# Performance work log

Hardware: AMD Instinct MI355X
Metric: run time of the kernel (lower is better)

## Reference

```python
import jax, jax.numpy as jnp
import numpy as np

DIM = 512
HEADS = 8
DIM_HEAD = 64
SCALE = DIM_HEAD ** -0.5


def setup_inputs() -> dict:
    key = jax.random.key(0)
    k1, k2, k3, k4, k5 = jax.random.split(key, 5)
    inner = HEADS * DIM_HEAD
    x = jax.random.normal(k1, (16, DIM, 32, 32), dtype=jnp.float32)
    W_proj = jax.random.normal(k2, (DIM, inner * 3), dtype=jnp.float32) * (DIM ** -0.5)
    b_proj = jax.random.normal(k3, (inner * 3,), dtype=jnp.float32) * 0.01
    W_out = jax.random.normal(k4, (inner, DIM), dtype=jnp.float32) * (inner ** -0.5)
    b_out = jax.random.normal(k5, (DIM,), dtype=jnp.float32) * 0.01
    return {"x": x, "W_proj": W_proj, "b_proj": b_proj, "W_out": W_out, "b_out": b_out}


def reference(x, W_proj, b_proj, W_out, b_out):
    b, c, hh, ww = x.shape
    s = hh * ww
    xs = x.reshape(b, c, s).transpose(0, 2, 1)  # b s c
    qkv = xs @ W_proj + b_proj                  # b s (heads * 3*dim_head)
    qkv = qkv.reshape(b, s, HEADS, 3 * DIM_HEAD)
    q, k, v = jnp.split(qkv, 3, axis=-1)        # each: b s h d
    w = jnp.einsum('bshd,bthd->bsth', q, k) * SCALE
    w = jax.nn.softmax(w, axis=2)
    res = jnp.einsum('bsth,bthd->bshd', w, v).reshape(b, s, HEADS * DIM_HEAD)
    out = res @ W_out + b_out + xs              # b s c (residual)
    return out.transpose(0, 2, 1).reshape(b, c, hh, ww)
```

## Files before the change

### kernel.cpp

```cpp
#include <hip/hip_runtime.h>
#include <hip/hip_bf16.h>

#define BATCH 16
#define CDIM  512
#define SEQ   1024
#define HEADS 8
#define DHEAD 64
#define N3    1536
#define QSCALE 0.18033688011112042f

typedef unsigned short ushort_t;
typedef __attribute__((ext_vector_type(8))) short short8;
typedef __attribute__((ext_vector_type(4))) float f32x4;

__device__ __forceinline__ unsigned f2bf(float f) {
    unsigned u = __float_as_uint(f);
    u += 0x7fffu + ((u >> 16) & 1u);
    return u >> 16;
}
__device__ __forceinline__ float fast_exp2(float x) {
    float r;
    asm("v_exp_f32 %0, %1" : "=v"(r) : "v"(x));
    return r;
}
__device__ __forceinline__ unsigned pack_bf16_trunc(float lo, float hi) {
    return __builtin_amdgcn_perm(__float_as_uint(hi), __float_as_uint(lo), 0x07060302u);
}
__device__ __forceinline__ void async16(const void* g, void* l) {
    __builtin_amdgcn_global_load_lds(
        (const __attribute__((address_space(1))) unsigned int*)g,
        (__attribute__((address_space(3))) unsigned int*)l, 16, 0, 0);
}


__global__ __launch_bounds__(256) void blockify_kernel(
    const float* __restrict__ in, ushort_t* __restrict__ out, int C)
{
    __shared__ float t[64][65];
    const int k0 = blockIdx.y * 64, c0 = blockIdx.x * 64;
    const float* inb = in + (size_t)blockIdx.z * 512 * C;
    const int tid = threadIdx.x;
#pragma unroll
    for (int i = 0; i < 16; ++i) {
        int idx = tid + i * 256;
        int r = idx >> 6, c = idx & 63;
        t[r][c] = inb[(size_t)(k0 + r) * C + c0 + c];
    }
    __syncthreads();
    const size_t mbase = (size_t)blockIdx.z * C + c0;
    const int ml = tid & 63;
#pragma unroll
    for (int i = 0; i < 2; ++i) {
        int oct = (tid >> 6) + i * 4;
        size_t m = mbase + ml;
        int mt = (int)(m >> 7), mr = (int)(m & 127);
        int m16 = mr >> 4, col = mr & 15;
        int k = k0 + oct * 8;
        int it = k >> 5, q = (k >> 3) & 3;
        uint4 pk;
        pk.x = f2bf(t[oct * 8 + 0][ml]) | (f2bf(t[oct * 8 + 1][ml]) << 16);
        pk.y = f2bf(t[oct * 8 + 2][ml]) | (f2bf(t[oct * 8 + 3][ml]) << 16);
        pk.z = f2bf(t[oct * 8 + 4][ml]) | (f2bf(t[oct * 8 + 5][ml]) << 16);
        pk.w = f2bf(t[oct * 8 + 6][ml]) | (f2bf(t[oct * 8 + 7][ml]) << 16);
        size_t off = ((size_t)(mt * 16 + it) * 8 + m16) * 512 + (q * 16 + col) * 8;
        *(uint4*)&out[off] = pk;
    }
}

__global__ __launch_bounds__(256) void qkv_gemm_kernel(
    const ushort_t* __restrict__ xtb, const ushort_t* __restrict__ WpTb,
    const float* __restrict__ bp,
    ushort_t* __restrict__ q_buf, ushort_t* __restrict__ kb,
    ushort_t* __restrict__ vb)
{
    __shared__ alignas(16) ushort_t Asub[2][8 * 512];
    __shared__ alignas(16) ushort_t Bsub[2][8 * 512];

    const int tid = threadIdx.x, w = tid >> 6, lane = tid & 63;
    const int quad = lane >> 4, col = lane & 15;
    const int wm = w >> 1, wn = w & 1;

    const int lin = blockIdx.x + 12 * blockIdx.y;
    const int xcd = lin & 7;
    const int rr  = lin >> 3;
    const int n0  = (rr % 12) * 128;
    const int m0  = ((rr / 12) * 8 + xcd) * 128;

    f32x4 acc[4][4];
#pragma unroll
    for (int i = 0; i < 4; ++i)
#pragma unroll
        for (int j = 0; j < 4; ++j) acc[i][j] = (f32x4){0.f, 0.f, 0.f, 0.f};

    const ushort_t* Ab = xtb  + (size_t)(m0 >> 7) * 65536 + (w * 2) * 512 + lane * 8;
    const ushort_t* Bb = WpTb + (size_t)(n0 >> 7) * 65536 + (w * 2) * 512 + lane * 8;

#define QKV_STAGE(buf, it)                                        \
    do {                                                          \
        async16(Ab + (it) * 4096,       &Asub[buf][(w * 2 + 0) * 512]); \
        async16(Ab + (it) * 4096 + 512, &Asub[buf][(w * 2 + 1) * 512]); \
        async16(Bb + (it) * 4096,       &Bsub[buf][(w * 2 + 0) * 512]); \
        async16(Bb + (it) * 4096 + 512, &Bsub[buf][(w * 2 + 1) * 512]); \
    } while (0)

    QKV_STAGE(0, 0);
    for (int it = 0; it < 16; ++it) {
        const int cur = it & 1;
        __syncthreads();
        if (it < 15) QKV_STAGE(cur ^ 1, it + 1);

        short8 af[4], bfr[4];
#pragma unroll
        for (int i = 0; i < 4; ++i) af[i]  = *(const short8*)&Asub[cur][(wm * 4 + i) * 512 + lane * 8];
#pragma unroll
        for (int j = 0; j < 4; ++j) bfr[j] = *(const short8*)&Bsub[cur][(wn * 4 + j) * 512 + lane * 8];
#pragma unroll
        for (int i = 0; i < 4; ++i)
#pragma unroll
            for (int j = 0; j < 4; ++j)
                acc[i][j] = __builtin_amdgcn_mfma_f32_16x16x32_bf16(af[i], bfr[j], acc[i][j], 0, 0, 0);
    }
#undef QKV_STAGE

    const int b = m0 >> 10, s0 = m0 & 1023;
    const size_t b8 = (size_t)b * HEADS;
#pragma unroll
    for (int j = 0; j < 4; ++j) {
        int nb = n0 + wn * 64 + j * 16;
        int h = nb / 192, rem = nb % 192;
        int type = rem >> 6, dbase = rem & 63;
        float bias = bp[nb + col];
        size_t bh = b8 + h;
        int d = dbase + col;
#pragma unroll
        for (int i = 0; i < 4; ++i) {
            int sb = s0 + wm * 64 + i * 16 + quad * 4;
            f32x4 v = acc[i][j];
            if (type == 2) {
                unsigned lo = f2bf(v[0] + bias) | (f2bf(v[1] + bias) << 16);
                unsigned hi = f2bf(v[2] + bias) | (f2bf(v[3] + bias) << 16);
                uint2 pk; pk.x = lo; pk.y = hi;
                int itv = sb >> 6, sub = (d >> 4) * 2 + ((sb >> 5) & 1);
                size_t off = ((bh * 16 + itv) * 8 + sub) * 512
                           + (((sb >> 3) & 3) * 16 + (d & 15)) * 8 + (sb & 7);
                *(uint2*)&vb[off] = pk;
            } else if (type == 1) {
#pragma unroll
                for (int r = 0; r < 4; ++r) {
                    int t = sb + r;
                    int itk = t >> 6, sub = ((t >> 4) & 3) * 2 + (d >> 5);
                    size_t off = ((bh * 16 + itk) * 8 + sub) * 512
                               + (((d >> 3) & 3) * 16 + (t & 15)) * 8 + (d & 7);
                    kb[off] = (ushort_t)f2bf(v[r] + bias);
                }
            } else {
#pragma unroll
                for (int r = 0; r < 4; ++r)
                    q_buf[(bh * SEQ + sb + r) * DHEAD + d] =
                        (ushort_t)f2bf((v[r] + bias) * QSCALE);
            }
        }
    }
}

__global__ __launch_bounds__(256) void attn_kernel(
    const ushort_t* __restrict__ q_buf, const ushort_t* __restrict__ kb,
    const ushort_t* __restrict__ vb, ushort_t* __restrict__ resb)
{
    __shared__ alignas(16) ushort_t Kf[2][8 * 512];
    __shared__ alignas(16) ushort_t Vf[2][8 * 512];
    __shared__ alignas(16) ushort_t Pf[4 * 1024];

    const int tid  = threadIdx.x;
    const int w    = tid >> 6;
    const int lane = tid & 63;
    const int quad = lane >> 4;
    const int col  = lane & 15;

    const int bhid = blockIdx.x;
    const int b = bhid >> 3, h = bhid & 7;
    const int q0 = blockIdx.y * 128;
    const size_t bh = (size_t)b * HEADS + h;

    const ushort_t* qp = q_buf + ((bh * SEQ) + q0 + w * 32 + col) * DHEAD + quad * 8;
    short8 qf0[2], qf1[2];
    qf0[0] = *(const short8*)(qp);
    qf1[0] = *(const short8*)(qp + 32);
    qf0[1] = *(const short8*)(qp + 16 * DHEAD);
    qf1[1] = *(const short8*)(qp + 16 * DHEAD + 32);

    short8 ones;
#pragma unroll
    for (int i = 0; i < 8; ++i) ones[i] = (short)0x3F80;

    f32x4 O[2][4];
#pragma unroll
    for (int g = 0; g < 2; ++g)
#pragma unroll
        for (int i = 0; i < 4; ++i) O[g][i] = (f32x4){0.f, 0.f, 0.f, 0.f};
    f32x4 L[2];
    L[0] = (f32x4){0.f, 0.f, 0.f, 0.f};
    L[1] = (f32x4){0.f, 0.f, 0.f, 0.f};

    const ushort_t* kaB = kb + (size_t)bh * 65536 + (w * 2) * 512 + lane * 8;
    const ushort_t* vaB = vb + (size_t)bh * 65536 + (w * 2) * 512 + lane * 8;

    const int poff_base = col * 8 + (quad & 1) * 4;
    const int qh = quad >> 1;
    ushort_t* pg = &Pf[w * 1024];

    async16(kaB,       &Kf[0][(w * 2 + 0) * 512]);
    async16(kaB + 512, &Kf[0][(w * 2 + 1) * 512]);
    async16(vaB,       &Vf[0][(w * 2 + 0) * 512]);
    async16(vaB + 512, &Vf[0][(w * 2 + 1) * 512]);
    kaB += 4096;
    vaB += 4096;

    for (int it = 0; it < 16; ++it) {
        const int cur = it & 1;
        const ushort_t* kc = Kf[cur];
        const ushort_t* vc = Vf[cur];
        __syncthreads();
        if (it < 15) {
            async16(kaB,       &Kf[cur ^ 1][(w * 2 + 0) * 512]);
            async16(kaB + 512, &Kf[cur ^ 1][(w * 2 + 1) * 512]);
            async16(vaB,       &Vf[cur ^ 1][(w * 2 + 0) * 512]);
            async16(vaB + 512, &Vf[cur ^ 1][(w * 2 + 1) * 512]);
            kaB += 4096;
            vaB += 4096;
        }

        f32x4 S[2][4];
#pragma unroll
        for (int t16 = 0; t16 < 4; ++t16) {
            const short8 k0 = *(const short8*)&kc[(t16 * 2 + 0) * 512 + lane * 8];
            const short8 k1 = *(const short8*)&kc[(t16 * 2 + 1) * 512 + lane * 8];
#pragma unroll
            for (int g = 0; g < 2; ++g) {
                f32x4 a = (f32x4){0.f, 0.f, 0.f, 0.f};
                a = __builtin_amdgcn_mfma_f32_16x16x32_bf16(k0, qf0[g], a, 0, 0, 0);
                a = __builtin_amdgcn_mfma_f32_16x16x32_bf16(k1, qf1[g], a, 0, 0, 0);
                S[g][t16] = a;
            }
        }

        short8 pf[2][2];
#pragma unroll
        for (int g = 0; g < 2; ++g) {
#pragma unroll
            for (int t16 = 0; t16 < 4; ++t16) {
                uint2 pk;
                pk.x = pack_bf16_trunc(fast_exp2(S[g][t16][0]), fast_exp2(S[g][t16][1]));
                pk.y = pack_bf16_trunc(fast_exp2(S[g][t16][2]), fast_exp2(S[g][t16][3]));
                int off = (t16 >> 1) * 512 + (((t16 * 2) + qh) & 3) * 128 + poff_base;
                *(uint2*)&pg[off] = pk;
            }
            pf[g][0] = *(const short8*)&pg[lane * 8];
            pf[g][1] = *(const short8*)&pg[512 + lane * 8];
        }

#pragma unroll
        for (int d16 = 0; d16 < 4; ++d16) {
            const short8 v0 = *(const short8*)&vc[(d16 * 2 + 0) * 512 + lane * 8];
            const short8 v1 = *(const short8*)&vc[(d16 * 2 + 1) * 512 + lane * 8];
#pragma unroll
            for (int g = 0; g < 2; ++g) {
                O[g][d16] = __builtin_amdgcn_mfma_f32_16x16x32_bf16(pf[g][0], v0, O[g][d16], 0, 0, 0);
                O[g][d16] = __builtin_amdgcn_mfma_f32_16x16x32_bf16(pf[g][1], v1, O[g][d16], 0, 0, 0);
            }
        }
#pragma unroll
        for (int g = 0; g < 2; ++g) {
            L[g] = __builtin_amdgcn_mfma_f32_16x16x32_bf16(pf[g][0], ones, L[g], 0, 0, 0);
            L[g] = __builtin_amdgcn_mfma_f32_16x16x32_bf16(pf[g][1], ones, L[g], 0, 0, 0);
        }
    }

    const int mt = b * 8 + (q0 >> 7);
#pragma unroll
    for (int g = 0; g < 2; ++g) {
        const int m16 = w * 2 + g;
#pragma unroll
        for (int r = 0; r < 4; ++r) {
            float inv = 1.f / L[g][r];
            const int mcol = quad * 4 + r;
#pragma unroll
            for (int d16 = 0; d16 < 4; ++d16) {
                int itk = h * 2 + (d16 >> 1);
                int kq = (d16 & 1) * 2 + (col >> 3);
                size_t off = ((size_t)(mt * 16 + itk) * 8 + m16) * 512
                           + (kq * 16 + mcol) * 8 + (col & 7);
                resb[off] = (ushort_t)f2bf(O[g][d16][r] * inv);
            }
        }
    }
}

__global__ __launch_bounds__(256) void out_gemm_kernel(
    const ushort_t* __restrict__ resb, const ushort_t* __restrict__ WoTb,
    const float* __restrict__ bo, const float* __restrict__ x,
    float* __restrict__ out)
{
    __shared__ alignas(16) ushort_t Asub[2][8 * 512];
    __shared__ alignas(16) ushort_t Bsub[2][8 * 512];

    const int tid = threadIdx.x, w = tid >> 6, lane = tid & 63;
    const int quad = lane >> 4, col = lane & 15;
    const int wm = w >> 1, wn = w & 1;

    const int lin = blockIdx.x + 4 * blockIdx.y;
    const int xcd = lin & 7;
    const int rr  = lin >> 3;
    const int n0  = (rr & 3) * 128;
    const int m0  = ((rr >> 2) * 8 + xcd) * 128;

    f32x4 acc[4][4];
#pragma unroll
    for (int i = 0; i < 4; ++i)
#pragma unroll
        for (int j = 0; j < 4; ++j) acc[i][j] = (f32x4){0.f, 0.f, 0.f, 0.f};

    const ushort_t* Ab = resb + (size_t)(m0 >> 7) * 65536 + (w * 2) * 512 + lane * 8;
    const ushort_t* Bb = WoTb + (size_t)(n0 >> 7) * 65536 + (w * 2) * 512 + lane * 8;

#define OUT_STAGE(buf, it)                                        \
    do {                                                          \
        async16(Ab + (it) * 4096,       &Asub[buf][(w * 2 + 0) * 512]); \
        async16(Ab + (it) * 4096 + 512, &Asub[buf][(w * 2 + 1) * 512]); \
        async16(Bb + (it) * 4096,       &Bsub[buf][(w * 2 + 0) * 512]); \
        async16(Bb + (it) * 4096 + 512, &Bsub[buf][(w * 2 + 1) * 512]); \
    } while (0)

    OUT_STAGE(0, 0);
    for (int it = 0; it < 16; ++it) {
        const int cur = it & 1;
        __syncthreads();
        if (it < 15) OUT_STAGE(cur ^ 1, it + 1);

        short8 af[4], bfr[4];
#pragma unroll
        for (int i = 0; i < 4; ++i) af[i]  = *(const short8*)&Asub[cur][(wm * 4 + i) * 512 + lane * 8];
#pragma unroll
        for (int j = 0; j < 4; ++j) bfr[j] = *(const short8*)&Bsub[cur][(wn * 4 + j) * 512 + lane * 8];
#pragma unroll
        for (int i = 0; i < 4; ++i)
#pragma unroll
            for (int j = 0; j < 4; ++j)
                acc[i][j] = __builtin_amdgcn_mfma_f32_16x16x32_bf16(af[i], bfr[j], acc[i][j], 0, 0, 0);
    }
#undef OUT_STAGE

    const int b = m0 >> 10, s0 = m0 & 1023;
#pragma unroll
    for (int j = 0; j < 4; ++j) {
        int n = n0 + wn * 64 + j * 16 + col;
        float bias = bo[n];
#pragma unroll
        for (int i = 0; i < 4; ++i) {
            int sb = s0 + wm * 64 + i * 16 + quad * 4;
            size_t o = ((size_t)b * CDIM + n) * SEQ + sb;
            float4 xr = *(const float4*)&x[o];
            f32x4 v = acc[i][j];
            float4 ov;
            ov.x = v[0] + bias + xr.x;
            ov.y = v[1] + bias + xr.y;
            ov.z = v[2] + bias + xr.z;
            ov.w = v[3] + bias + xr.w;
            *(float4*)&out[o] = ov;
        }
    }
}

extern "C" void kernel_launch(void* const* d_in, const int* in_sizes, int n_in,
                              void* d_out, int out_size, void* d_ws, size_t ws_size,
                              hipStream_t stream) {
    const float* x  = (const float*)d_in[0];
    const float* Wp = (const float*)d_in[1];
    const float* bp = (const float*)d_in[2];
    const float* Wo = (const float*)d_in[3];
    const float* bo = (const float*)d_in[4];
    float* out = (float*)d_out;

    ushort_t* xtb   = (ushort_t*)d_ws;
    ushort_t* WpTb  = xtb   + (size_t)8388608;
    ushort_t* WoTb  = WpTb  + (size_t)786432;
    ushort_t* q_buf = WoTb  + (size_t)262144;
    ushort_t* kb    = q_buf + (size_t)8388608;
    ushort_t* vb    = kb    + (size_t)8388608;
    ushort_t* resb  = vb    + (size_t)8388608;

    blockify_kernel<<<dim3(16, 8, 16), 256, 0, stream>>>(x,  xtb,  1024);
    blockify_kernel<<<dim3(24, 8, 1),  256, 0, stream>>>(Wp, WpTb, 1536);
    blockify_kernel<<<dim3(8, 8, 1),   256, 0, stream>>>(Wo, WoTb, 512);
    qkv_gemm_kernel<<<dim3(12, 128), 256, 0, stream>>>(xtb, WpTb, bp, q_buf, kb, vb);
    attn_kernel<<<dim3(128, 8), 256, 0, stream>>>(q_buf, kb, vb, resb);
    out_gemm_kernel<<<dim3(4, 128), 256, 0, stream>>>(resb, WoTb, bo, x, out);
}
```

Before: 202.9 us.

## Use two waves per attention block, each handling 64 queries

The attention kernel now runs with 128 threads (2 waves) instead of 256. Each wave processes four 16-row query groups instead of two, so every K and V fragment read from LDS feeds twice as many MFMAs. K fragments are hoisted into registers once per tile. s_setprio hints are added around the MFMA bursts. The cost is higher register pressure from doubled accumulators and fewer waves per block to hide latency, and each wave now issues twice as many async copies per stage.

```diff
diff --git a/kernel.cpp b/kernel.cpp
--- a/kernel.cpp
+++ b/kernel.cpp
@@ -163,13 +163,13 @@
     }
 }
 
-__global__ __launch_bounds__(256) void attn_kernel(
+__global__ __launch_bounds__(128) void attn_kernel(
     const ushort_t* __restrict__ q_buf, const ushort_t* __restrict__ kb,
     const ushort_t* __restrict__ vb, ushort_t* __restrict__ resb)
 {
     __shared__ alignas(16) ushort_t Kf[2][8 * 512];
     __shared__ alignas(16) ushort_t Vf[2][8 * 512];
-    __shared__ alignas(16) ushort_t Pf[4 * 1024];
+    __shared__ alignas(16) ushort_t Pf[2 * 1024];
 
     const int tid  = threadIdx.x;
     const int w    = tid >> 6;
@@ -182,76 +182,82 @@
     const int q0 = blockIdx.y * 128;
     const size_t bh = (size_t)b * HEADS + h;
 
-    const ushort_t* qp = q_buf + ((bh * SEQ) + q0 + w * 32 + col) * DHEAD + quad * 8;
-    short8 qf0[2], qf1[2];
-    qf0[0] = *(const short8*)(qp);
-    qf1[0] = *(const short8*)(qp + 32);
-    qf0[1] = *(const short8*)(qp + 16 * DHEAD);
-    qf1[1] = *(const short8*)(qp + 16 * DHEAD + 32);
+    const ushort_t* qp = q_buf + ((bh * SEQ) + q0 + w * 64 + col) * DHEAD + quad * 8;
+    short8 qf0[4], qf1[4];
+#pragma unroll
+    for (int g = 0; g < 4; ++g) {
+        qf0[g] = *(const short8*)(qp + g * 16 * DHEAD);
+        qf1[g] = *(const short8*)(qp + g * 16 * DHEAD + 32);
+    }
 
     short8 ones;
 #pragma unroll
     for (int i = 0; i < 8; ++i) ones[i] = (short)0x3F80;
 
-    f32x4 O[2][4];
-#pragma unroll
-    for (int g = 0; g < 2; ++g)
+    f32x4 O[4][4];
+#pragma unroll
+    for (int g = 0; g < 4; ++g)
 #pragma unroll
         for (int i = 0; i < 4; ++i) O[g][i] = (f32x4){0.f, 0.f, 0.f, 0.f};
-    f32x4 L[2];
-    L[0] = (f32x4){0.f, 0.f, 0.f, 0.f};
-    L[1] = (f32x4){0.f, 0.f, 0.f, 0.f};
-
-    const ushort_t* kaB = kb + (size_t)bh * 65536 + (w * 2) * 512 + lane * 8;
-    const ushort_t* vaB = vb + (size_t)bh * 65536 + (w * 2) * 512 + lane * 8;
+    f32x4 L[4];
+#pragma unroll
+    for (int g = 0; g < 4; ++g) L[g] = (f32x4){0.f, 0.f, 0.f, 0.f};
+
+    const ushort_t* kaB = kb + (size_t)bh * 65536 + (w * 4) * 512 + lane * 8;
+    const ushort_t* vaB = vb + (size_t)bh * 65536 + (w * 4) * 512 + lane * 8;
 
     const int poff_base = col * 8 + (quad & 1) * 4;
     const int qh = quad >> 1;
     ushort_t* pg = &Pf[w * 1024];
 
-    async16(kaB,       &Kf[0][(w * 2 + 0) * 512]);
-    async16(kaB + 512, &Kf[0][(w * 2 + 1) * 512]);
-    async16(vaB,       &Vf[0][(w * 2 + 0) * 512]);
-    async16(vaB + 512, &Vf[0][(w * 2 + 1) * 512]);
-    kaB += 4096;
-    vaB += 4096;
+#define ATTN_STAGE(buf)                                            \
+    do {                                                           \
+        async16(kaB,        &Kf[buf][(w * 4 + 0) * 512]);          \
+        async16(kaB + 512,  &Kf[buf][(w * 4 + 1) * 512]);          \
+        async16(kaB + 1024, &Kf[buf][(w * 4 + 2) * 512]);          \
+        async16(kaB + 1536, &Kf[buf][(w * 4 + 3) * 512]);          \
+        async16(vaB,        &Vf[buf][(w * 4 + 0) * 512]);          \
+        async16(vaB + 512,  &Vf[buf][(w * 4 + 1) * 512]);          \
+        async16(vaB + 1024, &Vf[buf][(w * 4 + 2) * 512]);          \
+        async16(vaB + 1536, &Vf[buf][(w * 4 + 3) * 512]);          \
+        kaB += 4096;                                               \
+        vaB += 4096;                                               \
+    } while (0)
+
+    ATTN_STAGE(0);
 
     for (int it = 0; it < 16; ++it) {
         const int cur = it & 1;
         const ushort_t* kc = Kf[cur];
         const ushort_t* vc = Vf[cur];
         __syncthreads();
-        if (it < 15) {
-            async16(kaB,       &Kf[cur ^ 1][(w * 2 + 0) * 512]);
-            async16(kaB + 512, &Kf[cur ^ 1][(w * 2 + 1) * 512]);
-            async16(vaB,       &Vf[cur ^ 1][(w * 2 + 0) * 512]);
-            async16(vaB + 512, &Vf[cur ^ 1][(w * 2 + 1) * 512]);
-            kaB += 4096;
-            vaB += 4096;
-        }
-
-        f32x4 S[2][4];
+        if (it < 15) ATTN_STAGE(cur ^ 1);
+
+        short8 kf[8];
 #pragma unroll
         for (int t16 = 0; t16 < 4; ++t16) {
-            const short8 k0 = *(const short8*)&kc[(t16 * 2 + 0) * 512 + lane * 8];
-            const short8 k1 = *(const short8*)&kc[(t16 * 2 + 1) * 512 + lane * 8];
-#pragma unroll
-            for (int g = 0; g < 2; ++g) {
+            kf[2 * t16 + 0] = *(const short8*)&kc[(t16 * 2 + 0) * 512 + lane * 8];
+            kf[2 * t16 + 1] = *(const short8*)&kc[(t16 * 2 + 1) * 512 + lane * 8];
+        }
+
+        short8 pf[4][2];
+#pragma unroll
+        for (int g = 0; g < 4; ++g) {
+            f32x4 S[4];
+            __builtin_amdgcn_s_setprio(1);
+#pragma unroll
+            for (int t16 = 0; t16 < 4; ++t16) {
                 f32x4 a = (f32x4){0.f, 0.f, 0.f, 0.f};
-                a = __builtin_amdgcn_mfma_f32_16x16x32_bf16(k0, qf0[g], a, 0, 0, 0);
-                a = __builtin_amdgcn_mfma_f32_16x16x32_bf16(k1, qf1[g], a, 0, 0, 0);
-                S[g][t16] = a;
+                a = __builtin_amdgcn_mfma_f32_16x16x32_bf16(kf[2 * t16 + 0], qf0[g], a, 0, 0, 0);
+                a = __builtin_amdgcn_mfma_f32_16x16x32_bf16(kf[2 * t16 + 1], qf1[g], a, 0, 0, 0);
+                S[t16] = a;
             }
-        }
-
-        short8 pf[2][2];
-#pragma unroll
-        for (int g = 0; g < 2; ++g) {
+            __builtin_amdgcn_s_setprio(0);
 #pragma unroll
             for (int t16 = 0; t16 < 4; ++t16) {
                 uint2 pk;
-                pk.x = pack_bf16_trunc(fast_exp2(S[g][t16][0]), fast_exp2(S[g][t16][1]));
-                pk.y = pack_bf16_trunc(fast_exp2(S[g][t16][2]), fast_exp2(S[g][t16][3]));
+                pk.x = pack_bf16_trunc(fast_exp2(S[t16][0]), fast_exp2(S[t16][1]));
+                pk.y = pack_bf16_trunc(fast_exp2(S[t16][2]), fast_exp2(S[t16][3]));
                 int off = (t16 >> 1) * 512 + (((t16 * 2) + qh) & 3) * 128 + poff_base;
                 *(uint2*)&pg[off] = pk;
             }
@@ -263,23 +269,26 @@
         for (int d16 = 0; d16 < 4; ++d16) {
             const short8 v0 = *(const short8*)&vc[(d16 * 2 + 0) * 512 + lane * 8];
             const short8 v1 = *(const short8*)&vc[(d16 * 2 + 1) * 512 + lane * 8];
-#pragma unroll
-            for (int g = 0; g < 2; ++g) {
+            __builtin_amdgcn_s_setprio(1);
+#pragma unroll
+            for (int g = 0; g < 4; ++g) {
                 O[g][d16] = __builtin_amdgcn_mfma_f32_16x16x32_bf16(pf[g][0], v0, O[g][d16], 0, 0, 0);
                 O[g][d16] = __builtin_amdgcn_mfma_f32_16x16x32_bf16(pf[g][1], v1, O[g][d16], 0, 0, 0);
             }
-        }
-#pragma unroll
-        for (int g = 0; g < 2; ++g) {
+            __builtin_amdgcn_s_setprio(0);
+        }
+#pragma unroll
+        for (int g = 0; g < 4; ++g) {
             L[g] = __builtin_amdgcn_mfma_f32_16x16x32_bf16(pf[g][0], ones, L[g], 0, 0, 0);
             L[g] = __builtin_amdgcn_mfma_f32_16x16x32_bf16(pf[g][1], ones, L[g], 0, 0, 0);
         }
     }
+#undef ATTN_STAGE
 
     const int mt = b * 8 + (q0 >> 7);
 #pragma unroll
-    for (int g = 0; g < 2; ++g) {
-        const int m16 = w * 2 + g;
+    for (int g = 0; g < 4; ++g) {
+        const int m16 = w * 4 + g;
 #pragma unroll
         for (int r = 0; r < 4; ++r) {
             float inv = 1.f / L[g][r];
@@ -393,6 +402,6 @@
     blockify_kernel<<<dim3(24, 8, 1),  256, 0, stream>>>(Wp, WpTb, 1536);
     blockify_kernel<<<dim3(8, 8, 1),   256, 0, stream>>>(Wo, WoTb, 512);
     qkv_gemm_kernel<<<dim3(12, 128), 256, 0, stream>>>(xtb, WpTb, bp, q_buf, kb, vb);
-    attn_kernel<<<dim3(128, 8), 256, 0, stream>>>(q_buf, kb, vb, resb);
+    attn_kernel<<<dim3(128, 8), 128, 0, stream>>>(q_buf, kb, vb, resb);
     out_gemm_kernel<<<dim3(4, 128), 256, 0, stream>>>(resb, WoTb, bo, x, out);
 }
```

Measured after the change: 195.0 us. 3.9% less time.
